# Kernel tuning notes

Hardware: AMD Instinct MI355X
Metric: run time of the kernel (lower is better)

## Reference

```python
import jax, jax.numpy as jnp
import numpy as np

B, S, D, M, E, K = 4, 1024, 2048, 512, 8, 2
AUX_W = 0.01


def setup_inputs() -> dict:
    key = jax.random.key(0)
    ks = jax.random.split(key, 9)
    n = lambda k, sh, fan: jax.random.normal(k, sh, jnp.float32) * (fan ** -0.5)
    return {
        "hidden_states": jax.random.normal(ks[0], (B, S, D), jnp.float32),
        "w_router": n(ks[1], (D, E), D),
        "wi0": n(ks[2], (E, D, M), D),
        "wi1": n(ks[3], (E, D, M), D),
        "wo": n(ks[4], (E, M, D), M),
        "sw_wi0": n(ks[5], (D, M), D),
        "sw_wi1": n(ks[6], (D, M), D),
        "sw_wo": n(ks[7], (M, D), M),
        "w_shared_gate": n(ks[8], (D, 1), D),
        "deterministic": 1,
    }


def reference(hidden_states, w_router, wi0, wi1, wo, sw_wi0, sw_wi1, sw_wo, w_shared_gate, deterministic):
    b, s, d = hidden_states.shape
    x = hidden_states.reshape(-1, d)  # [T, D]
    T = x.shape[0]

    # --- router: softmax over experts, top-k, renormalize top-k weights ---
    logits = (x @ w_router).astype(jnp.float32)           # [T, E]
    probs = jax.nn.softmax(logits, axis=-1)
    top_w, top_i = jax.lax.top_k(probs, K)                # [T, K]
    top_w = top_w / jnp.sum(top_w, axis=-1, keepdims=True)
    one_hot = jax.nn.one_hot(top_i, E, dtype=probs.dtype)  # [T, K, E]
    combine = jnp.einsum("tk,tke->te", top_w, one_hot)     # [T, E] sparse combine weights

    # --- load-balance aux loss (MaxText style) ---
    density = jnp.mean(jnp.sum(one_hot, axis=1), axis=0)    # fraction routed per expert
    density_proxy = jnp.mean(probs, axis=0)                 # mean router prob per expert
    load_balance_loss = jnp.mean(density * density_proxy) * (E * E) * AUX_W

    # --- routed experts: scan over experts, gated MLP, weighted combine ---
    def expert_step(acc, packed):
        wi0_e, wi1_e, wo_e, w_e = packed  # [D,M],[D,M],[M,D],[T]
        h = jax.nn.silu(x @ wi0_e) * (x @ wi1_e)            # [T, M]
        return acc + w_e[:, None] * (h @ wo_e), None

    routed, _ = jax.lax.scan(
        expert_step, jnp.zeros_like(x), (wi0, wi1, wo, combine.T)
    )

    # --- shared expert (gated MLP) + sigmoid shared gate ---
    hs = jax.nn.silu(x @ sw_wi0) * (x @ sw_wi1)
    shared = hs @ sw_wo                                     # [T, D]
    gate = jax.nn.sigmoid(x @ w_shared_gate)                # [T, 1]

    out = (routed + gate * shared).reshape(b, s, d)
    return out, load_balance_loss
```

## Files before the change

### kernel.cpp

```cpp
#include <hip/hip_runtime.h>
#include <hip/hip_bf16.h>
#include <math.h>

#define TT 4096
#define DD 2048
#define MM 512
#define EE 8

typedef __attribute__((ext_vector_type(8))) short short8;
typedef __attribute__((ext_vector_type(4))) float f32x4;

__device__ __forceinline__ unsigned short f2bf(float f) {
  union { float f; unsigned u; } v; v.f = f;
  unsigned u = v.u;
  unsigned r = u + 0x7FFFu + ((u >> 16) & 1u);
  return (unsigned short)(r >> 16);
}

__device__ __forceinline__ float bf2f(unsigned short u) {
  union { unsigned u; float f; } v; v.u = ((unsigned)u) << 16;
  return v.f;
}

__device__ __forceinline__ int imin(int a, int b) { return a < b ? a : b; }

__device__ __forceinline__ void gld16(const void* g, void* l) {
  __builtin_amdgcn_global_load_lds(
      (const __attribute__((address_space(1))) void*)g,
      (__attribute__((address_space(3))) void*)l, 16, 0, 0);
}

__global__ __launch_bounds__(256) void prep_kernel(
    const float* __restrict__ wi0, const float* __restrict__ wi1,
    const float* __restrict__ wo, const float* __restrict__ swi0,
    const float* __restrict__ swi1, const float* __restrict__ swo,
    unsigned short* __restrict__ wi0T, unsigned short* __restrict__ wi1T,
    unsigned short* __restrict__ woT, unsigned short* __restrict__ swi0T,
    unsigned short* __restrict__ swi1T, unsigned short* __restrict__ swoT,
    const float* __restrict__ x, const float* __restrict__ wr,
    const float* __restrict__ wg, unsigned short* __restrict__ xb,
    int* __restrict__ topk_i, float* __restrict__ topk_w,
    float* __restrict__ gate, int* __restrict__ cnt, float* __restrict__ proxy)
{
  __shared__ unsigned short st[64][72];
  __shared__ float s_proxy[EE];
  __shared__ int s_cnt[EE];
  int b = blockIdx.x;
  int tid = threadIdx.x;

  if (b < 27 * 64) {
    int slice = b >> 6, q = b & 63;
    const float* s; unsigned short* d;
    int R, C, tcb;
    if (slice < 8)       { s = wi0 + (size_t)slice * DD * MM;        d = wi0T + (size_t)slice * DD * MM;        R = DD; C = MM; tcb = 3; }
    else if (slice < 16) { s = wi1 + (size_t)(slice - 8) * DD * MM;  d = wi1T + (size_t)(slice - 8) * DD * MM;  R = DD; C = MM; tcb = 3; }
    else if (slice < 24) { s = wo + (size_t)(slice - 16) * MM * DD;  d = woT + (size_t)(slice - 16) * MM * DD;  R = MM; C = DD; tcb = 5; }
    else if (slice == 24){ s = swi0; d = swi0T; R = DD; C = MM; tcb = 3; }
    else if (slice == 25){ s = swi1; d = swi1T; R = DD; C = MM; tcb = 3; }
    else                 { s = swo;  d = swoT;  R = MM; C = DD; tcb = 5; }
    int ncmask = (1 << tcb) - 1;
    int tr = tid >> 4;
    int tc4 = (tid & 15) * 4;
    int orow = tid >> 2;
    int oc = (tid & 3) * 16;

    float4 cur[4], nxt[4];
    int t0 = q * 4;
    int c0 = (t0 & ncmask) * 64, r0 = (t0 >> tcb) * 64;
#pragma unroll
    for (int i = 0; i < 4; ++i)
      cur[i] = *(const float4*)&s[(size_t)(r0 + tr + i * 16) * C + (c0 + tc4)];

    for (int k = 0; k < 4; ++k) {
      int nr0 = 0, nc0 = 0;
      if (k < 3) {
        int t = q * 4 + k + 1;
        nc0 = (t & ncmask) * 64; nr0 = (t >> tcb) * 64;
#pragma unroll
        for (int i = 0; i < 4; ++i)
          nxt[i] = *(const float4*)&s[(size_t)(nr0 + tr + i * 16) * C + (nc0 + tc4)];
      }
      __builtin_amdgcn_s_barrier();
#pragma unroll
      for (int i = 0; i < 4; ++i) {
        int r = tr + i * 16;
        st[r][tc4 + 0] = f2bf(cur[i].x); st[r][tc4 + 1] = f2bf(cur[i].y);
        st[r][tc4 + 2] = f2bf(cur[i].z); st[r][tc4 + 3] = f2bf(cur[i].w);
      }
      asm volatile("s_waitcnt lgkmcnt(0)" ::: "memory");
      __builtin_amdgcn_s_barrier();
      short8 v0, v1;
#pragma unroll
      for (int j = 0; j < 8; ++j) { v0[j] = st[oc + j][orow]; v1[j] = st[oc + 8 + j][orow]; }
      *(short8*)&d[(size_t)(c0 + orow) * R + (r0 + oc)] = v0;
      *(short8*)&d[(size_t)(c0 + orow) * R + (r0 + oc + 8)] = v1;
      if (k < 3) {
        r0 = nr0; c0 = nc0;
#pragma unroll
        for (int i = 0; i < 4; ++i) cur[i] = nxt[i];
      }
    }
    return;
  }

  int rb = b - 27 * 64;
  if (tid < EE) { s_proxy[tid] = 0.f; s_cnt[tid] = 0; }
  __syncthreads();
  int wave = tid >> 6, lane = tid & 63;
  int t = rb * 4 + wave;
  const float* xr = x + (size_t)t * DD;
  unsigned short* xbr = xb + (size_t)t * DD;
  float p[EE];
#pragma unroll
  for (int e = 0; e < EE; ++e) p[e] = 0.f;
  float pg = 0.f;
  for (int i = 0; i < DD / 64; ++i) {
    int d = lane + i * 64;
    float xv = xr[d];
    xbr[d] = f2bf(xv);
    const float* w = wr + d * EE;
#pragma unroll
    for (int e = 0; e < EE; ++e) p[e] = fmaf(xv, w[e], p[e]);
    pg = fmaf(xv, wg[d], pg);
  }
#pragma unroll
  for (int e = 0; e < EE; ++e) {
#pragma unroll
    for (int off = 32; off; off >>= 1) p[e] += __shfl_xor(p[e], off);
  }
#pragma unroll
  for (int off = 32; off; off >>= 1) pg += __shfl_xor(pg, off);

  if (lane == 0) {
    float mx = p[0];
#pragma unroll
    for (int e = 1; e < EE; ++e) mx = fmaxf(mx, p[e]);
    float pr[EE]; float s = 0.f;
#pragma unroll
    for (int e = 0; e < EE; ++e) { pr[e] = __expf(p[e] - mx); s += pr[e]; }
    float inv = 1.f / s;
#pragma unroll
    for (int e = 0; e < EE; ++e) pr[e] *= inv;
    int i0 = 0;
#pragma unroll
    for (int e = 1; e < EE; ++e) if (p[e] > p[i0]) i0 = e;
    int i1 = (i0 == 0) ? 1 : 0;
#pragma unroll
    for (int e = 0; e < EE; ++e) if (e != i0 && p[e] > p[i1]) i1 = e;
    float w0 = pr[i0], w1 = pr[i1], s2 = w0 + w1;
    topk_i[t * 2] = i0; topk_i[t * 2 + 1] = i1;
    topk_w[t * 2] = w0 / s2; topk_w[t * 2 + 1] = w1 / s2;
    gate[t] = 1.f / (1.f + __expf(-pg));
    atomicAdd(&s_cnt[i0], 1);
    atomicAdd(&s_cnt[i1], 1);
#pragma unroll
    for (int e = 0; e < EE; ++e) atomicAdd(&s_proxy[e], pr[e]);
  }
  __syncthreads();
  if (tid < EE) {
    atomicAdd(&cnt[tid], s_cnt[tid]);
    atomicAdd(&proxy[tid], s_proxy[tid]);
  }
}

__global__ void offsets_loss_kernel(const int* __restrict__ cnt, int* __restrict__ offs,
                                    const float* __restrict__ proxy, float* __restrict__ out_loss)
{
  if (threadIdx.x == 0 && blockIdx.x == 0) {
    int acc = 0; float l = 0.f;
    for (int e = 0; e < EE; ++e) {
      offs[e] = acc; acc += cnt[e];
      l += (float)cnt[e] * proxy[e];
    }
    out_loss[0] = l * (0.01f * (float)EE) / ((float)TT * (float)TT);
  }
}

__global__ void fill_kernel(const int* __restrict__ topk_i,
                            const int* __restrict__ offs, int* __restrict__ fillc,
                            int* __restrict__ btok, int* __restrict__ slotOf)
{
  int idx = blockIdx.x * blockDim.x + threadIdx.x;
  if (idx >= TT * 2) return;
  int e = topk_i[idx];
  int slot = atomicAdd(&fillc[e], 1);
  int p = offs[e] + slot;
  btok[p] = idx >> 1;
  slotOf[idx] = p;
}

__global__ __launch_bounds__(256) void gemm1_kernel(
    const unsigned short* __restrict__ xb,
    const unsigned short* __restrict__ wi0T, const unsigned short* __restrict__ wi1T,
    const unsigned short* __restrict__ swi0T, const unsigned short* __restrict__ swi1T,
    unsigned short* __restrict__ H, unsigned short* __restrict__ Hs,
    const int* __restrict__ btok, const int* __restrict__ cnt, const int* __restrict__ offs)
{
  __shared__ __align__(16) unsigned short lA[128 * 64];
  __shared__ __align__(16) unsigned short lB[128 * 64];
  int z = blockIdx.z;
  const unsigned short *w0, *w1;
  const int* tok = nullptr;
  unsigned short* Ho;
  int n;
  if (z < EE) {
    n = cnt[z];
    int rb = offs[z];
    tok = btok + rb;
    w0 = wi0T + (size_t)z * (DD * MM);
    w1 = wi1T + (size_t)z * (DD * MM);
    Ho = H + (size_t)rb * MM;
  } else { n = TT; w0 = swi0T; w1 = swi1T; Ho = Hs; }
  int row0 = blockIdx.y * 128;
  if (row0 >= n) return;
  int m0 = blockIdx.x * 64;
  int tid = threadIdx.x, lane = tid & 63, wv = tid >> 6;

  int lsub = lane >> 3;
  int chl = (lane & 7) ^ lsub;

  const unsigned short* gA[4];
  const unsigned short* gB[4];
#pragma unroll
  for (int c = 0; c < 4; ++c) {
    int row = c * 32 + wv * 8 + lsub;
    int tr;
    if (tok) tr = tok[imin(row0 + row, n - 1)];
    else     tr = row0 + row;
    gA[c] = xb + (size_t)tr * DD + chl * 8;
    int mat = row >> 6, col = row & 63;
    const unsigned short* wsel = mat ? w1 : w0;
    gB[c] = wsel + (size_t)(m0 + col) * DD + chl * 8;
  }

  int rw = (wv & 1) * 64;
  int cg = (wv >> 1) * 32;
  int fr = lane & 15;
  int grp = lane >> 4;
  int lr4 = (lane >> 4) * 4, lc = lane & 15;

  f32x4 acc[4][4];
  f32x4 zf = {0.f, 0.f, 0.f, 0.f};
#pragma unroll
  for (int i = 0; i < 4; ++i)
#pragma unroll
    for (int c = 0; c < 4; ++c) acc[i][c] = zf;

  for (int k0 = 0; k0 < DD; k0 += 64) {
    __syncthreads();
#pragma unroll
    for (int c = 0; c < 4; ++c) gld16(gA[c] + k0, lA + c * 2048 + wv * 512);
#pragma unroll
    for (int c = 0; c < 4; ++c) gld16(gB[c] + k0, lB + c * 2048 + wv * 512);
    __syncthreads();
#pragma unroll
    for (int s = 0; s < 2; ++s) {
      int cq = s * 4 + grp;
      short8 af[4], bf[4];
#pragma unroll
      for (int i = 0; i < 4; ++i) {
        int row = rw + i * 16 + fr;
        af[i] = *(const short8*)&lA[row * 64 + ((cq ^ (row & 7)) * 8)];
      }
#pragma unroll
      for (int c = 0; c < 4; ++c) {
        int rowb = (c >> 1) * 64 + cg + (c & 1) * 16 + fr;
        bf[c] = *(const short8*)&lB[rowb * 64 + ((cq ^ (rowb & 7)) * 8)];
      }
#pragma unroll
      for (int i = 0; i < 4; ++i)
#pragma unroll
        for (int c = 0; c < 4; ++c)
          acc[i][c] = __builtin_amdgcn_mfma_f32_16x16x32_bf16(af[i], bf[c], acc[i][c], 0, 0, 0);
    }
  }

#pragma unroll
  for (int i = 0; i < 4; ++i) {
#pragma unroll
    for (int c = 0; c < 2; ++c) {
#pragma unroll
      for (int rg = 0; rg < 4; ++rg) {
        int row = row0 + rw + i * 16 + lr4 + rg;
        if (row < n) {
          float a0 = acc[i][c][rg];
          float a1 = acc[i][c + 2][rg];
          float h = a0 / (1.f + __expf(-a0)) * a1;
          Ho[(size_t)row * MM + m0 + cg + c * 16 + lc] = f2bf(h);
        }
      }
    }
  }
}

__global__ __launch_bounds__(256) void gemm2_kernel(
    const unsigned short* __restrict__ H, const unsigned short* __restrict__ Hs,
    const unsigned short* __restrict__ woT, const unsigned short* __restrict__ swoT,
    unsigned short* __restrict__ Yr, unsigned short* __restrict__ Ys,
    const int* __restrict__ cnt, const int* __restrict__ offs)
{
  __shared__ __align__(16) unsigned short lA[128 * 64];
  __shared__ __align__(16) unsigned short lB[128 * 64];
  int z = blockIdx.z;
  int n, rb;
  const unsigned short *Hb, *wb;
  unsigned short* Yd;
  if (z < EE) { n = cnt[z]; rb = offs[z]; Hb = H + (size_t)rb * MM; wb = woT + (size_t)z * (DD * MM); Yd = Yr + (size_t)rb * DD; }
  else        { n = TT; rb = 0; Hb = Hs; wb = swoT; Yd = Ys; }
  int row0 = blockIdx.y * 128;
  if (row0 >= n) return;
  int d0 = blockIdx.x * 128;
  int tid = threadIdx.x, lane = tid & 63, wv = tid >> 6;

  int lsub = lane >> 3;
  int chl = (lane & 7) ^ lsub;

  const unsigned short* gA[4];
  const unsigned short* gB[4];
#pragma unroll
  for (int c = 0; c < 4; ++c) {
    int row = c * 32 + wv * 8 + lsub;
    int sr = imin(row0 + row, n - 1);
    gA[c] = Hb + (size_t)sr * MM + chl * 8;
    gB[c] = wb + (size_t)(d0 + row) * MM + chl * 8;
  }

  int rw = (wv & 1) * 64;
  int cw = (wv >> 1) * 64;
  int fr = lane & 15;
  int grp = lane >> 4;
  int lr4 = (lane >> 4) * 4, lc = lane & 15;

  f32x4 acc[4][4];
  f32x4 zf = {0.f, 0.f, 0.f, 0.f};
#pragma unroll
  for (int i = 0; i < 4; ++i)
#pragma unroll
    for (int c = 0; c < 4; ++c) acc[i][c] = zf;

  for (int k0 = 0; k0 < MM; k0 += 64) {
    __syncthreads();
#pragma unroll
    for (int c = 0; c < 4; ++c) gld16(gA[c] + k0, lA + c * 2048 + wv * 512);
#pragma unroll
    for (int c = 0; c < 4; ++c) gld16(gB[c] + k0, lB + c * 2048 + wv * 512);
    __syncthreads();
#pragma unroll
    for (int s = 0; s < 2; ++s) {
      int cq = s * 4 + grp;
      short8 af[4], bf[4];
#pragma unroll
      for (int i = 0; i < 4; ++i) {
        int row = rw + i * 16 + fr;
        af[i] = *(const short8*)&lA[row * 64 + ((cq ^ (row & 7)) * 8)];
      }
#pragma unroll
      for (int c = 0; c < 4; ++c) {
        int rowb = cw + c * 16 + fr;
        bf[c] = *(const short8*)&lB[rowb * 64 + ((cq ^ (rowb & 7)) * 8)];
      }
#pragma unroll
      for (int i = 0; i < 4; ++i)
#pragma unroll
        for (int c = 0; c < 4; ++c)
          acc[i][c] = __builtin_amdgcn_mfma_f32_16x16x32_bf16(af[i], bf[c], acc[i][c], 0, 0, 0);
    }
  }

#pragma unroll
  for (int i = 0; i < 4; ++i) {
#pragma unroll
    for (int c = 0; c < 4; ++c) {
#pragma unroll
      for (int rg = 0; rg < 4; ++rg) {
        int row = row0 + rw + i * 16 + lr4 + rg;
        if (row < n)
          Yd[(size_t)row * DD + d0 + cw + c * 16 + lc] = f2bf(acc[i][c][rg]);
      }
    }
  }
}

__global__ __launch_bounds__(256) void combine_kernel(
    const unsigned short* __restrict__ Yr, const unsigned short* __restrict__ Ys,
    const int* __restrict__ slotOf, const float* __restrict__ topk_w,
    const float* __restrict__ gate, float* __restrict__ out)
{
  int t = blockIdx.x;
  int d0 = threadIdx.x * 8;
  int p0 = slotOf[t * 2], p1 = slotOf[t * 2 + 1];
  float w0 = topk_w[t * 2], w1 = topk_w[t * 2 + 1], g = gate[t];
  short8 a = *(const short8*)&Yr[(size_t)p0 * DD + d0];
  short8 b = *(const short8*)&Yr[(size_t)p1 * DD + d0];
  short8 s = *(const short8*)&Ys[(size_t)t * DD + d0];
  float r[8];
#pragma unroll
  for (int j = 0; j < 8; ++j)
    r[j] = w0 * bf2f((unsigned short)a[j]) + w1 * bf2f((unsigned short)b[j])
         + g * bf2f((unsigned short)s[j]);
  float4 o0 = {r[0], r[1], r[2], r[3]};
  float4 o1 = {r[4], r[5], r[6], r[7]};
  float* op = out + (size_t)t * DD + d0;
  *(float4*)op = o0;
  *(float4*)(op + 4) = o1;
}

extern "C" void kernel_launch(void* const* d_in, const int* in_sizes, int n_in,
                              void* d_out, int out_size, void* d_ws, size_t ws_size,
                              hipStream_t stream) {
  const float* x    = (const float*)d_in[0];
  const float* wr   = (const float*)d_in[1];
  const float* wi0  = (const float*)d_in[2];
  const float* wi1  = (const float*)d_in[3];
  const float* wo   = (const float*)d_in[4];
  const float* swi0 = (const float*)d_in[5];
  const float* swi1 = (const float*)d_in[6];
  const float* swo  = (const float*)d_in[7];
  const float* wg   = (const float*)d_in[8];
  float* out = (float*)d_out;

  char* ws = (char*)d_ws;
  int*   cnt    = (int*)(ws + 0);
  int*   fillc  = (int*)(ws + 64);
  int*   offs   = (int*)(ws + 128);
  float* proxy  = (float*)(ws + 192);
  int*   topk_i = (int*)(ws + 1024);
  float* topk_w = (float*)(ws + 33792);
  int*   btok   = (int*)(ws + 66560);
  float* gate   = (float*)(ws + 132096);
  int*   slotOf = (int*)(ws + 148480);
  unsigned short* xb    = (unsigned short*)(ws + 1048576);
  unsigned short* H     = (unsigned short*)(ws + 17825792);
  unsigned short* Hs    = (unsigned short*)(ws + 26214400);
  unsigned short* wi0T  = (unsigned short*)(ws + 30408704);
  unsigned short* wi1T  = (unsigned short*)(ws + 47185920);
  unsigned short* woT   = (unsigned short*)(ws + 63963136);
  unsigned short* swi0T = (unsigned short*)(ws + 80740352);
  unsigned short* swi1T = (unsigned short*)(ws + 82837504);
  unsigned short* swoT  = (unsigned short*)(ws + 84934656);
  unsigned short* Ys = xb;
  unsigned short* Yr = wi0T;

  hipMemsetAsync(ws, 0, 256, stream);

  prep_kernel<<<27 * 64 + TT / 4, 256, 0, stream>>>(
      wi0, wi1, wo, swi0, swi1, swo, wi0T, wi1T, woT, swi0T, swi1T, swoT,
      x, wr, wg, xb, topk_i, topk_w, gate, cnt, proxy);
  offsets_loss_kernel<<<1, 64, 0, stream>>>(cnt, offs, proxy, out + (size_t)TT * DD);
  fill_kernel<<<(TT * 2) / 256, 256, 0, stream>>>(topk_i, offs, fillc, btok, slotOf);

  gemm1_kernel<<<dim3(MM / 64, 32, EE + 1), 256, 0, stream>>>(
      xb, wi0T, wi1T, swi0T, swi1T, H, Hs, btok, cnt, offs);
  gemm2_kernel<<<dim3(DD / 128, 32, EE + 1), 256, 0, stream>>>(
      H, Hs, woT, swoT, Yr, Ys, cnt, offs);
  combine_kernel<<<TT, 256, 0, stream>>>(Yr, Ys, slotOf, topk_w, gate, out);
}
```

Before: 224.2 us.

## Double-buffer LDS tiles in both expert GEMMs to overlap loads with MFMA

Both GEMM kernels now keep two LDS buffers per operand and prefetch the next K tile into the spare buffer while computing on the current one. This replaces two barriers per iteration with one. MFMA sections are also wrapped in s_setprio to favour the math waves. LDS use doubles to 64KB per block, which may lower occupancy. If gld16 is a synchronous global-to-register-to-LDS copy, the overlap depends on how the compiler schedules it.

```diff
diff --git a/kernel.cpp b/kernel.cpp
--- a/kernel.cpp
+++ b/kernel.cpp
@@ -196,8 +196,8 @@
     unsigned short* __restrict__ H, unsigned short* __restrict__ Hs,
     const int* __restrict__ btok, const int* __restrict__ cnt, const int* __restrict__ offs)
 {
-  __shared__ __align__(16) unsigned short lA[128 * 64];
-  __shared__ __align__(16) unsigned short lB[128 * 64];
+  __shared__ __align__(16) unsigned short lA[2][128 * 64];
+  __shared__ __align__(16) unsigned short lB[2][128 * 64];
   int z = blockIdx.z;
   const unsigned short *w0, *w1;
   const int* tok = nullptr;
@@ -246,13 +246,23 @@
 #pragma unroll
     for (int c = 0; c < 4; ++c) acc[i][c] = zf;
 
+#pragma unroll
+  for (int c = 0; c < 4; ++c) gld16(gA[c], lA[0] + c * 2048 + wv * 512);
+#pragma unroll
+  for (int c = 0; c < 4; ++c) gld16(gB[c], lB[0] + c * 2048 + wv * 512);
+  __syncthreads();
+
+  int cur = 0;
   for (int k0 = 0; k0 < DD; k0 += 64) {
-    __syncthreads();
-#pragma unroll
-    for (int c = 0; c < 4; ++c) gld16(gA[c] + k0, lA + c * 2048 + wv * 512);
-#pragma unroll
-    for (int c = 0; c < 4; ++c) gld16(gB[c] + k0, lB + c * 2048 + wv * 512);
-    __syncthreads();
+    int nk = k0 + 64;
+    if (nk < DD) {
+#pragma unroll
+      for (int c = 0; c < 4; ++c) gld16(gA[c] + nk, lA[cur ^ 1] + c * 2048 + wv * 512);
+#pragma unroll
+      for (int c = 0; c < 4; ++c) gld16(gB[c] + nk, lB[cur ^ 1] + c * 2048 + wv * 512);
+    }
+    const unsigned short* la = lA[cur];
+    const unsigned short* lb = lB[cur];
 #pragma unroll
     for (int s = 0; s < 2; ++s) {
       int cq = s * 4 + grp;
@@ -260,19 +270,23 @@
 #pragma unroll
       for (int i = 0; i < 4; ++i) {
         int row = rw + i * 16 + fr;
-        af[i] = *(const short8*)&lA[row * 64 + ((cq ^ (row & 7)) * 8)];
+        af[i] = *(const short8*)&la[row * 64 + ((cq ^ (row & 7)) * 8)];
       }
 #pragma unroll
       for (int c = 0; c < 4; ++c) {
         int rowb = (c >> 1) * 64 + cg + (c & 1) * 16 + fr;
-        bf[c] = *(const short8*)&lB[rowb * 64 + ((cq ^ (rowb & 7)) * 8)];
-      }
+        bf[c] = *(const short8*)&lb[rowb * 64 + ((cq ^ (rowb & 7)) * 8)];
+      }
+      __builtin_amdgcn_s_setprio(1);
 #pragma unroll
       for (int i = 0; i < 4; ++i)
 #pragma unroll
         for (int c = 0; c < 4; ++c)
           acc[i][c] = __builtin_amdgcn_mfma_f32_16x16x32_bf16(af[i], bf[c], acc[i][c], 0, 0, 0);
-    }
+      __builtin_amdgcn_s_setprio(0);
+    }
+    if (nk < DD) __syncthreads();
+    cur ^= 1;
   }
 
 #pragma unroll
@@ -299,8 +313,8 @@
     unsigned short* __restrict__ Yr, unsigned short* __restrict__ Ys,
     const int* __restrict__ cnt, const int* __restrict__ offs)
 {
-  __shared__ __align__(16) unsigned short lA[128 * 64];
-  __shared__ __align__(16) unsigned short lB[128 * 64];
+  __shared__ __align__(16) unsigned short lA[2][128 * 64];
+  __shared__ __align__(16) unsigned short lB[2][128 * 64];
   int z = blockIdx.z;
   int n, rb;
   const unsigned short *Hb, *wb;
@@ -338,13 +352,23 @@
 #pragma unroll
     for (int c = 0; c < 4; ++c) acc[i][c] = zf;
 
+#pragma unroll
+  for (int c = 0; c < 4; ++c) gld16(gA[c], lA[0] + c * 2048 + wv * 512);
+#pragma unroll
+  for (int c = 0; c < 4; ++c) gld16(gB[c], lB[0] + c * 2048 + wv * 512);
+  __syncthreads();
+
+  int cur = 0;
   for (int k0 = 0; k0 < MM; k0 += 64) {
-    __syncthreads();
-#pragma unroll
-    for (int c = 0; c < 4; ++c) gld16(gA[c] + k0, lA + c * 2048 + wv * 512);
-#pragma unroll
-    for (int c = 0; c < 4; ++c) gld16(gB[c] + k0, lB + c * 2048 + wv * 512);
-    __syncthreads();
+    int nk = k0 + 64;
+    if (nk < MM) {
+#pragma unroll
+      for (int c = 0; c < 4; ++c) gld16(gA[c] + nk, lA[cur ^ 1] + c * 2048 + wv * 512);
+#pragma unroll
+      for (int c = 0; c < 4; ++c) gld16(gB[c] + nk, lB[cur ^ 1] + c * 2048 + wv * 512);
+    }
+    const unsigned short* la = lA[cur];
+    const unsigned short* lb = lB[cur];
 #pragma unroll
     for (int s = 0; s < 2; ++s) {
       int cq = s * 4 + grp;
@@ -352,19 +376,23 @@
 #pragma unroll
       for (int i = 0; i < 4; ++i) {
         int row = rw + i * 16 + fr;
-        af[i] = *(const short8*)&lA[row * 64 + ((cq ^ (row & 7)) * 8)];
+        af[i] = *(const short8*)&la[row * 64 + ((cq ^ (row & 7)) * 8)];
       }
 #pragma unroll
       for (int c = 0; c < 4; ++c) {
         int rowb = cw + c * 16 + fr;
-        bf[c] = *(const short8*)&lB[rowb * 64 + ((cq ^ (rowb & 7)) * 8)];
-      }
+        bf[c] = *(const short8*)&lb[rowb * 64 + ((cq ^ (rowb & 7)) * 8)];
+      }
+      __builtin_amdgcn_s_setprio(1);
 #pragma unroll
       for (int i = 0; i < 4; ++i)
 #pragma unroll
         for (int c = 0; c < 4; ++c)
           acc[i][c] = __builtin_amdgcn_mfma_f32_16x16x32_bf16(af[i], bf[c], acc[i][c], 0, 0, 0);
-    }
+      __builtin_amdgcn_s_setprio(0);
+    }
+    if (nk < MM) __syncthreads();
+    cur ^= 1;
   }
 
 #pragma unroll
```

Measured after the change: 239.8 us. 6.9% more time.

## Double-buffer LDS tiles in both expert GEMM kernels to overlap loads with MFMA

Applied to the files above, without the earlier changes.

Both GEMM kernels now use two LDS buffers for the A and B tiles. The next K-slice is issued with async global-to-LDS loads while the current slice is computed, and each step needs one barrier instead of two. The goal is to hide global load latency behind MFMA work. In exchange, LDS use per block doubles (64KB), which may lower occupancy.

```diff
diff --git a/kernel.cpp b/kernel.cpp
--- a/kernel.cpp
+++ b/kernel.cpp
@@ -196,8 +196,10 @@
     unsigned short* __restrict__ H, unsigned short* __restrict__ Hs,
     const int* __restrict__ btok, const int* __restrict__ cnt, const int* __restrict__ offs)
 {
-  __shared__ __align__(16) unsigned short lA[128 * 64];
-  __shared__ __align__(16) unsigned short lB[128 * 64];
+  __shared__ __align__(16) unsigned short lA0[128 * 64];
+  __shared__ __align__(16) unsigned short lA1[128 * 64];
+  __shared__ __align__(16) unsigned short lB0[128 * 64];
+  __shared__ __align__(16) unsigned short lB1[128 * 64];
   int z = blockIdx.z;
   const unsigned short *w0, *w1;
   const int* tok = nullptr;
@@ -246,13 +248,13 @@
 #pragma unroll
     for (int c = 0; c < 4; ++c) acc[i][c] = zf;
 
-  for (int k0 = 0; k0 < DD; k0 += 64) {
-    __syncthreads();
-#pragma unroll
-    for (int c = 0; c < 4; ++c) gld16(gA[c] + k0, lA + c * 2048 + wv * 512);
-#pragma unroll
-    for (int c = 0; c < 4; ++c) gld16(gB[c] + k0, lB + c * 2048 + wv * 512);
-    __syncthreads();
+  auto stage = [&](int kk, unsigned short* la, unsigned short* lb) {
+#pragma unroll
+    for (int c = 0; c < 4; ++c) gld16(gA[c] + kk, la + c * 2048 + wv * 512);
+#pragma unroll
+    for (int c = 0; c < 4; ++c) gld16(gB[c] + kk, lb + c * 2048 + wv * 512);
+  };
+  auto compute = [&](const unsigned short* la, const unsigned short* lb) {
 #pragma unroll
     for (int s = 0; s < 2; ++s) {
       int cq = s * 4 + grp;
@@ -260,12 +262,12 @@
 #pragma unroll
       for (int i = 0; i < 4; ++i) {
         int row = rw + i * 16 + fr;
-        af[i] = *(const short8*)&lA[row * 64 + ((cq ^ (row & 7)) * 8)];
+        af[i] = *(const short8*)&la[row * 64 + ((cq ^ (row & 7)) * 8)];
       }
 #pragma unroll
       for (int c = 0; c < 4; ++c) {
         int rowb = (c >> 1) * 64 + cg + (c & 1) * 16 + fr;
-        bf[c] = *(const short8*)&lB[rowb * 64 + ((cq ^ (rowb & 7)) * 8)];
+        bf[c] = *(const short8*)&lb[rowb * 64 + ((cq ^ (rowb & 7)) * 8)];
       }
 #pragma unroll
       for (int i = 0; i < 4; ++i)
@@ -273,7 +275,24 @@
         for (int c = 0; c < 4; ++c)
           acc[i][c] = __builtin_amdgcn_mfma_f32_16x16x32_bf16(af[i], bf[c], acc[i][c], 0, 0, 0);
     }
-  }
+  };
+
+  stage(0, lA0, lB0);
+  __syncthreads();
+
+  int k0 = 0;
+  for (; k0 < DD - 128; k0 += 128) {
+    stage(k0 + 64, lA1, lB1);
+    compute(lA0, lB0);
+    __syncthreads();
+    stage(k0 + 128, lA0, lB0);
+    compute(lA1, lB1);
+    __syncthreads();
+  }
+  stage(k0 + 64, lA1, lB1);
+  compute(lA0, lB0);
+  __syncthreads();
+  compute(lA1, lB1);
 
 #pragma unroll
   for (int i = 0; i < 4; ++i) {
@@ -299,8 +318,10 @@
     unsigned short* __restrict__ Yr, unsigned short* __restrict__ Ys,
     const int* __restrict__ cnt, const int* __restrict__ offs)
 {
-  __shared__ __align__(16) unsigned short lA[128 * 64];
-  __shared__ __align__(16) unsigned short lB[128 * 64];
+  __shared__ __align__(16) unsigned short lA0[128 * 64];
+  __shared__ __align__(16) unsigned short lA1[128 * 64];
+  __shared__ __align__(16) unsigned short lB0[128 * 64];
+  __shared__ __align__(16) unsigned short lB1[128 * 64];
   int z = blockIdx.z;
   int n, rb;
   const unsigned short *Hb, *wb;
@@ -338,13 +359,13 @@
 #pragma unroll
     for (int c = 0; c < 4; ++c) acc[i][c] = zf;
 
-  for (int k0 = 0; k0 < MM; k0 += 64) {
-    __syncthreads();
-#pragma unroll
-    for (int c = 0; c < 4; ++c) gld16(gA[c] + k0, lA + c * 2048 + wv * 512);
-#pragma unroll
-    for (int c = 0; c < 4; ++c) gld16(gB[c] + k0, lB + c * 2048 + wv * 512);
-    __syncthreads();
+  auto stage = [&](int kk, unsigned short* la, unsigned short* lb) {
+#pragma unroll
+    for (int c = 0; c < 4; ++c) gld16(gA[c] + kk, la + c * 2048 + wv * 512);
+#pragma unroll
+    for (int c = 0; c < 4; ++c) gld16(gB[c] + kk, lb + c * 2048 + wv * 512);
+  };
+  auto compute = [&](const unsigned short* la, const unsigned short* lb) {
 #pragma unroll
     for (int s = 0; s < 2; ++s) {
       int cq = s * 4 + grp;
@@ -352,12 +373,12 @@
 #pragma unroll
       for (int i = 0; i < 4; ++i) {
         int row = rw + i * 16 + fr;
-        af[i] = *(const short8*)&lA[row * 64 + ((cq ^ (row & 7)) * 8)];
+        af[i] = *(const short8*)&la[row * 64 + ((cq ^ (row & 7)) * 8)];
       }
 #pragma unroll
       for (int c = 0; c < 4; ++c) {
         int rowb = cw + c * 16 + fr;
-        bf[c] = *(const short8*)&lB[rowb * 64 + ((cq ^ (rowb & 7)) * 8)];
+        bf[c] = *(const short8*)&lb[rowb * 64 + ((cq ^ (rowb & 7)) * 8)];
       }
 #pragma unroll
       for (int i = 0; i < 4; ++i)
@@ -365,7 +386,24 @@
         for (int c = 0; c < 4; ++c)
           acc[i][c] = __builtin_amdgcn_mfma_f32_16x16x32_bf16(af[i], bf[c], acc[i][c], 0, 0, 0);
     }
-  }
+  };
+
+  stage(0, lA0, lB0);
+  __syncthreads();
+
+  int k0 = 0;
+  for (; k0 < MM - 128; k0 += 128) {
+    stage(k0 + 64, lA1, lB1);
+    compute(lA0, lB0);
+    __syncthreads();
+    stage(k0 + 128, lA0, lB0);
+    compute(lA1, lB1);
+    __syncthreads();
+  }
+  stage(k0 + 64, lA1, lB1);
+  compute(lA0, lB0);
+  __syncthreads();
+  compute(lA1, lB1);
 
 #pragma unroll
   for (int i = 0; i < 4; ++i) {
```

New measurement: 218.4 us. 1.03x faster.
